# Optimization experiments

Hardware: AMD Instinct MI355X
Metric: run time of the kernel (lower is better)

Reference implementation:

```python
import jax, jax.numpy as jnp
import numpy as np

N_HEADS = 16


def setup_inputs() -> dict:
    key = jax.random.key(0)
    ks = jax.random.split(key, 5)
    E = 1024
    x = jax.random.normal(ks[0], (2, 2048, E), dtype=jnp.float32)
    s = 1.0 / np.sqrt(E)
    Wq = jax.random.normal(ks[1], (E, E), dtype=jnp.float32) * s
    Wk = jax.random.normal(ks[2], (E, E), dtype=jnp.float32) * s
    Wv = jax.random.normal(ks[3], (E, E), dtype=jnp.float32) * s
    Wo = jax.random.normal(ks[4], (E, E), dtype=jnp.float32) * s
    bo = jnp.zeros((E,), dtype=jnp.float32)
    return {"x": x, "Wq": Wq, "Wk": Wk, "Wv": Wv, "Wo": Wo, "bo": bo}


def reference(x, Wq, Wk, Wv, Wo, bo):
    B, S, E = x.shape
    H = N_HEADS
    D = E // H
    # project and split heads: [B, H, S, D]
    def split_heads(y):
        return y.reshape(B, S, H, D).transpose(0, 2, 1, 3)
    q = split_heads(x @ Wq)
    k = split_heads(x @ Wk)
    v = split_heads(x @ Wv)
    # full score matrix [B, H, S, S]
    scores = jnp.einsum('bhqd,bhkd->bhqk', q, k)
    causal = jnp.triu(jnp.ones((S, S), dtype=bool), k=1)
    scores = jnp.where(causal, -jnp.inf, scores)
    attn = jax.nn.softmax(scores / jnp.sqrt(jnp.float32(D)), axis=-1)
    # dropout rate is 0.0 -> identity
    ctx = jnp.einsum('bhqk,bhkd->bhqd', attn, v)
    ctx = ctx.transpose(0, 2, 1, 3).reshape(B, S, E)
    return ctx @ Wo + bo
```

## Files before the change

### kernel.cpp

```cpp
#include <hip/hip_runtime.h>
#include <stdint.h>


#define N_HEADS 16
#define HD 64
#define SEQ 2048
#define EMB 1024

typedef __attribute__((ext_vector_type(8))) short s16x8;
typedef __attribute__((ext_vector_type(4))) float f32x4;
typedef __attribute__((ext_vector_type(16))) float f32x16;

#define QSCALE 0.18033688f

__device__ __forceinline__ short f2b(float f) {
  union { float f; uint32_t u; } v; v.f = f;
  uint32_t u = v.u;
  u += 0x7fffu + ((u >> 16) & 1u);
  return (short)(u >> 16);
}

__device__ __forceinline__ uint32_t pk2(float a, float b) {
  union { float f; uint32_t u; } x, y; x.f = a; y.f = b;
  return ((x.u + 0x8000u) >> 16) | ((y.u + 0x8000u) & 0xffff0000u);
}

__device__ __forceinline__ float exp2a(float x) {
  float r; asm("v_exp_f32 %0, %1" : "=v"(r) : "v"(x)); return r;
}

__device__ __forceinline__ void gll16(const void* g, void* l) {
  __builtin_amdgcn_global_load_lds((const __attribute__((address_space(1))) void*)g,
                                   (__attribute__((address_space(3))) void*)l, 16, 0, 0);
}

#define SWZ(row, chunk) ((((row) * 8) + ((chunk) ^ ((row) & 7))) * 8)

__global__ __launch_bounds__(256) void k_prep(const float* __restrict__ x,
                                              const float* __restrict__ W0,
                                              const float* __restrict__ W1,
                                              const float* __restrict__ W2,
                                              const float* __restrict__ W3,
                                              short* __restrict__ xb,
                                              short* __restrict__ wt) {
  const int z = blockIdx.x, t = threadIdx.x;
  if (z < 4096) {
    int i = z * 256 + t;
    float4 v = ((const float4*)x)[i];
    short4 o;
    o.x = f2b(v.x); o.y = f2b(v.y); o.z = f2b(v.z); o.w = f2b(v.w);
    ((short4*)xb)[i] = o;
  } else {
    __shared__ float tile[32][33];
    int bz = z - 4096;
    int w = bz >> 10, rem = bz & 1023;
    int bn = (rem & 31) * 32, bk = (rem >> 5) * 32;
    const float* W = w == 0 ? W0 : w == 1 ? W1 : w == 2 ? W2 : W3;
    short* o = wt + (size_t)w * EMB * EMB;
    int tx = t & 31, ty = t >> 5;
    for (int i = ty; i < 32; i += 8)
      tile[i][tx] = W[(size_t)(bk + i) * EMB + bn + tx];
    __syncthreads();
    for (int i = ty; i < 32; i += 8)
      o[(size_t)(bn + i) * EMB + bk + tx] = f2b(tile[tx][i]);
  }
}

template <int MODE>
__global__ __launch_bounds__(256) void k_gemm(const short* __restrict__ A,
                                              const short* __restrict__ BT,
                                              void* __restrict__ outp,
                                              const float* __restrict__ bias) {
  constexpr bool SWAP = (MODE != 2);
  constexpr int MAIN = 4 * 4096;
  constexpr int EPIL = (MODE == 1) ? 0 : 128 * 132;
  constexpr int SMSZ = MAIN > EPIL ? MAIN : EPIL;
  __shared__ alignas(16) short smem[SMSZ];

  const int t = threadIdx.x;
  const int m0 = blockIdx.x * 128;
  const int n0 = blockIdx.y * 128;
  const int wave = t >> 6, lane = t & 63;
  const int wm = (wave >> 1) * 64, wn = (wave & 1) * 64;
  const int l31 = lane & 31, lh = lane >> 5;

  const int srow = lane >> 2;
  const int soff = ((lane & 3) ^ (srow & 3)) * 8;

  auto stage = [&](int kb, int p) {
    short* as = smem + p * 4096;
    short* bs = smem + 8192 + p * 4096;
#pragma unroll
    for (int i = 0; i < 2; i++) {
      int rb = wave * 32 + i * 16;
      gll16(A + (size_t)(m0 + rb + srow) * EMB + kb + soff, &as[rb * 32]);
      gll16(BT + (size_t)(n0 + rb + srow) * EMB + kb + soff, &bs[rb * 32]);
    }
  };
  auto frd = [&](const short* sb, int row, int kh) -> s16x8 {
    int c = kh * 2 + lh;
    return *(const s16x8*)&sb[row * 32 + ((c ^ (row & 3)) * 8)];
  };

  f32x16 acc[2][2] = {};
  int pb = 0;
  stage(0, 0);
  for (int kb = 0; kb < EMB; kb += 32) {
    __syncthreads();
    if (kb + 32 < EMB) stage(kb + 32, pb ^ 1);
    const short* as = smem + pb * 4096;
    const short* bs = smem + 8192 + pb * 4096;
    s16x8 af[2][2], bf[2][2];
#pragma unroll
    for (int mt = 0; mt < 2; mt++)
#pragma unroll
      for (int kh = 0; kh < 2; kh++) af[mt][kh] = frd(as, wm + mt * 32 + l31, kh);
#pragma unroll
    for (int nt = 0; nt < 2; nt++)
#pragma unroll
      for (int kh = 0; kh < 2; kh++) bf[nt][kh] = frd(bs, wn + nt * 32 + l31, kh);
#pragma unroll
    for (int mt = 0; mt < 2; mt++)
#pragma unroll
      for (int nt = 0; nt < 2; nt++)
#pragma unroll
        for (int kh = 0; kh < 2; kh++)
          acc[mt][nt] = SWAP
            ? __builtin_amdgcn_mfma_f32_32x32x16_bf16(bf[nt][kh], af[mt][kh], acc[mt][nt], 0, 0, 0)
            : __builtin_amdgcn_mfma_f32_32x32x16_bf16(af[mt][kh], bf[nt][kh], acc[mt][nt], 0, 0, 0);
    pb ^= 1;
  }

  if (MODE == 0) {
    __syncthreads();
    short* Vls = smem;
    const int wsel = blockIdx.y >> 3;
    const float qs = (wsel == 0) ? QSCALE : 1.0f;
    const int n0l = (blockIdx.y & 7) * 128;
#pragma unroll
    for (int mt = 0; mt < 2; mt++) {
      int mr = wm + mt * 32 + l31;
#pragma unroll
      for (int nt = 0; nt < 2; nt++)
#pragma unroll
        for (int g = 0; g < 4; g++) {
          uint2 w;
          w.x = pk2(acc[mt][nt][4 * g + 0] * qs, acc[mt][nt][4 * g + 1] * qs);
          w.y = pk2(acc[mt][nt][4 * g + 2] * qs, acc[mt][nt][4 * g + 3] * qs);
          *(uint2*)&Vls[mr * 132 + wn + nt * 32 + g * 8 + 4 * lh] = w;
        }
    }
    __syncthreads();
    short* ob = (short*)outp + (size_t)wsel * (4u * 1024 * 1024);
    const int bb = m0 >> 11, ss0 = m0 & (SEQ - 1);
#pragma unroll
    for (int i = 0; i < 8; i++) {
      int mrow = i * 16 + (t >> 4);
      int ncol = (t & 15) * 8;
      int e = n0l + ncol, hh = e >> 6, dd = e & 63;
      *(uint4*)&ob[(((size_t)(bb * N_HEADS + hh) * SEQ) + ss0 + mrow) * 64 + dd] =
          *(const uint4*)&Vls[mrow * 132 + ncol];
    }
  } else if (MODE == 2) {
    __syncthreads();
    short* Vls = smem;
#pragma unroll
    for (int nt = 0; nt < 2; nt++) {
      int nl = wn + nt * 32 + l31;
#pragma unroll
      for (int mt = 0; mt < 2; mt++)
#pragma unroll
        for (int g = 0; g < 4; g++) {
          uint2 w;
          w.x = pk2(acc[mt][nt][4 * g + 0], acc[mt][nt][4 * g + 1]);
          w.y = pk2(acc[mt][nt][4 * g + 2], acc[mt][nt][4 * g + 3]);
          *(uint2*)&Vls[nl * 132 + wm + mt * 32 + g * 8 + 4 * lh] = w;
        }
    }
    __syncthreads();
    short* obv = (short*)outp + (size_t)8 * 1024 * 1024;
    const int bb = m0 >> 11, ss0 = m0 & (SEQ - 1);
#pragma unroll
    for (int i = 0; i < 8; i++) {
      int nl = i * 16 + (t >> 4);
      int mc = (t & 15) * 8;
      int e = n0 + nl, hh = e >> 6, dd = e & 63;
      *(uint4*)&obv[((size_t)((bb * N_HEADS + hh) * HD + dd)) * SEQ + ss0 + mc] =
          *(const uint4*)&Vls[nl * 132 + mc];
    }
  } else {
    float* of = (float*)outp;
#pragma unroll
    for (int mt = 0; mt < 2; mt++) {
      int mg = m0 + wm + mt * 32 + l31;
#pragma unroll
      for (int nt = 0; nt < 2; nt++)
#pragma unroll
        for (int g = 0; g < 4; g++) {
          int ng = n0 + wn + nt * 32 + g * 8 + 4 * lh;
          f32x4 bv = *(const f32x4*)&bias[ng];
          f32x4 w;
          w[0] = acc[mt][nt][4 * g + 0] + bv[0];
          w[1] = acc[mt][nt][4 * g + 1] + bv[1];
          w[2] = acc[mt][nt][4 * g + 2] + bv[2];
          w[3] = acc[mt][nt][4 * g + 3] + bv[3];
          *(f32x4*)&of[(size_t)mg * EMB + ng] = w;
        }
    }
  }
}

__global__ __launch_bounds__(256) void k_attn(const short* __restrict__ Q,
                                              const short* __restrict__ K,
                                              const short* __restrict__ Vt,
                                              short* __restrict__ ctx) {
  __shared__ alignas(16) short UQP[64 * 72];
  __shared__ alignas(16) short Ks0[64 * 64], Ks1[64 * 64];
  __shared__ alignas(16) short Vs0[64 * 64], Vs1[64 * 64];

  const int t = threadIdx.x, wave = t >> 6, lane = t & 63;
  const int ml = lane & 15, quad = lane >> 4;
  const int bh = blockIdx.x;
  const int qb = 31 - (int)blockIdx.y;
  const size_t base = (size_t)bh * SEQ * HD;
  const int q0 = qb * 64, wq = q0 + wave * 16;

  const int sr = lane >> 3;
  const int sc = ((lane & 7) ^ sr) * 8;

#pragma unroll
  for (int i = 0; i < 2; i++) {
    int r8 = wave * 16 + i * 8;
    gll16(Q + base + (size_t)(q0 + r8 + sr) * HD + sc, &UQP[r8 * 64]);
  }
  auto stageKV = [&](int kt, short* kd, short* vd) {
    const int kbase = kt * 64;
#pragma unroll
    for (int i = 0; i < 2; i++) {
      int r8 = wave * 16 + i * 8;
      gll16(K + base + (size_t)(kbase + r8 + sr) * HD + sc, &kd[r8 * 64]);
      gll16(Vt + base + (size_t)(r8 + sr) * SEQ + kbase + sc, &vd[r8 * 64]);
    }
  };

  f32x4 cacc[4] = {};
  float li = 0.f;
  short* Pw = &UQP[wave * 16 * 72];

  stageKV(0, Ks0, Vs0);
  __syncthreads();

  s16x8 qf[2];
#pragma unroll
  for (int c = 0; c < 2; c++)
    qf[c] = *(const s16x8*)&UQP[SWZ(wave * 16 + ml, 4 * c + quad)];
  __syncthreads();

  auto tile_body = [&](int kt, const short* kd, const short* vd) {
    const int kbase = kt * 64;
    if (kbase > wq + 15) return;
    const bool diag = (kbase + 63 > wq);
    f32x4 st[4];
#pragma unroll
    for (int nt = 0; nt < 4; nt++) {
      int row = nt * 16 + ml;
      s16x8 kf0 = *(const s16x8*)&kd[SWZ(row, quad)];
      s16x8 kf1 = *(const s16x8*)&kd[SWZ(row, 4 + quad)];
      f32x4 z = {};
      z = __builtin_amdgcn_mfma_f32_16x16x32_bf16(kf0, qf[0], z, 0, 0, 0);
      st[nt] = __builtin_amdgcn_mfma_f32_16x16x32_bf16(kf1, qf[1], z, 0, 0, 0);
    }
    const int qg = wq + ml;
    float rsum = 0.f;
#pragma unroll
    for (int nt = 0; nt < 4; nt++) {
      float p0 = exp2a(st[nt][0]);
      float p1 = exp2a(st[nt][1]);
      float p2 = exp2a(st[nt][2]);
      float p3 = exp2a(st[nt][3]);
      if (diag) {
        int kk = kbase + nt * 16 + quad * 4;
        if (kk + 0 > qg) p0 = 0.f;
        if (kk + 1 > qg) p1 = 0.f;
        if (kk + 2 > qg) p2 = 0.f;
        if (kk + 3 > qg) p3 = 0.f;
      }
      rsum += (p0 + p1) + (p2 + p3);
      uint2 w; w.x = pk2(p0, p1); w.y = pk2(p2, p3);
      *(uint2*)&Pw[ml * 72 + nt * 16 + quad * 4] = w;
    }
    li += rsum;
    __builtin_amdgcn_wave_barrier();

    s16x8 pf[2];
#pragma unroll
    for (int c = 0; c < 2; c++)
      pf[c] = *(const s16x8*)&Pw[ml * 72 + c * 32 + quad * 8];
#pragma unroll
    for (int mt = 0; mt < 4; mt++) {
      int row = mt * 16 + ml;
      s16x8 vf0 = *(const s16x8*)&vd[SWZ(row, quad)];
      s16x8 vf1 = *(const s16x8*)&vd[SWZ(row, 4 + quad)];
      cacc[mt] = __builtin_amdgcn_mfma_f32_16x16x32_bf16(vf0, pf[0], cacc[mt], 0, 0, 0);
      cacc[mt] = __builtin_amdgcn_mfma_f32_16x16x32_bf16(vf1, pf[1], cacc[mt], 0, 0, 0);
    }
  };

  for (int kt = 0; kt <= qb; kt += 2) {
    if (kt + 1 <= qb) stageKV(kt + 1, Ks1, Vs1);
    tile_body(kt, Ks0, Vs0);
    __syncthreads();
    if (kt + 2 <= qb) stageKV(kt + 2, Ks0, Vs0);
    if (kt + 1 <= qb) tile_body(kt + 1, Ks1, Vs1);
    __syncthreads();
  }

  li += __shfl_xor(li, 16, 64);
  li += __shfl_xor(li, 32, 64);
  float inv = 1.0f / li;
#pragma unroll
  for (int mt = 0; mt < 4; mt++) {
    uint2 w;
    w.x = pk2(cacc[mt][0] * inv, cacc[mt][1] * inv);
    w.y = pk2(cacc[mt][2] * inv, cacc[mt][3] * inv);
    *(uint2*)&Pw[ml * 72 + mt * 16 + quad * 4] = w;
  }
  __builtin_amdgcn_wave_barrier();
  const int b = bh >> 4, h = bh & 15;
#pragma unroll
  for (int i = 0; i < 2; i++) {
    int row = i * 8 + (lane >> 3);
    int q = wq + row;
    size_t gbase = ((size_t)(b * SEQ + q)) * EMB + h * 64 + (lane & 7) * 8;
    *(uint4*)&ctx[gbase] = *(const uint4*)&Pw[row * 72 + (lane & 7) * 8];
  }
}

extern "C" void kernel_launch(void* const* d_in, const int* in_sizes, int n_in,
                              void* d_out, int out_size, void* d_ws, size_t ws_size,
                              hipStream_t stream) {
  const float* x  = (const float*)d_in[0];
  const float* Wq = (const float*)d_in[1];
  const float* Wk = (const float*)d_in[2];
  const float* Wv = (const float*)d_in[3];
  const float* Wo = (const float*)d_in[4];
  const float* bo = (const float*)d_in[5];
  float* out = (float*)d_out;

  short* ws = (short*)d_ws;
  short* xb  = ws;
  short* wt  = ws + (size_t)4 * 1024 * 1024;
  short* qkv = ws + (size_t)8 * 1024 * 1024;

  k_prep<<<8192, 256, 0, stream>>>(x, Wq, Wk, Wv, Wo, xb, wt);
  k_gemm<0><<<dim3(32, 16), 256, 0, stream>>>(xb, wt, qkv, nullptr);
  k_gemm<2><<<dim3(32, 8), 256, 0, stream>>>(xb, wt + (size_t)2 * 1024 * 1024, qkv, nullptr);
  k_attn<<<dim3(32, 32), 256, 0, stream>>>(qkv, qkv + (size_t)4 * 1024 * 1024,
                                           qkv + (size_t)8 * 1024 * 1024, xb);
  k_gemm<1><<<dim3(32, 8), 256, 0, stream>>>(xb, wt + (size_t)3 * 1024 * 1024, out, bo);
}
```

Before: 179.6 us.

## Fuse QKV projections into one launch and use 128-row query blocks in attention

Merges the Q/K projection GEMM and the transposed V projection GEMM into a single launch with 24 column blocks, choosing the MFMA operand order and epilogue per block at runtime. The attention kernel now uses 512 threads per block covering 128 query rows, so each staged K/V tile serves twice as many queries and the grid is halved. This cuts one kernel launch and halves the K/V reloads. In exchange there are fewer attention blocks to spread over the compute units, and the causal work per block is less even.

```diff
diff --git a/kernel.cpp b/kernel.cpp
--- a/kernel.cpp
+++ b/kernel.cpp
@@ -12,6 +12,8 @@
 typedef __attribute__((ext_vector_type(16))) float f32x16;
 
 #define QSCALE 0.18033688f
+
+template <bool B> struct BC { static constexpr bool value = B; };
 
 __device__ __forceinline__ short f2b(float f) {
   union { float f; uint32_t u; } v; v.f = f;
@@ -71,15 +73,15 @@
                                               const short* __restrict__ BT,
                                               void* __restrict__ outp,
                                               const float* __restrict__ bias) {
-  constexpr bool SWAP = (MODE != 2);
   constexpr int MAIN = 4 * 4096;
   constexpr int EPIL = (MODE == 1) ? 0 : 128 * 132;
   constexpr int SMSZ = MAIN > EPIL ? MAIN : EPIL;
   __shared__ alignas(16) short smem[SMSZ];
 
   const int t = threadIdx.x;
+  const int by = blockIdx.y;
   const int m0 = blockIdx.x * 128;
-  const int n0 = blockIdx.y * 128;
+  const short* Bp = BT + (size_t)by * (128 * EMB);
   const int wave = t >> 6, lane = t & 63;
   const int wm = (wave >> 1) * 64, wn = (wave & 1) * 64;
   const int l31 = lane & 31, lh = lane >> 5;
@@ -94,7 +96,7 @@
     for (int i = 0; i < 2; i++) {
       int rb = wave * 32 + i * 16;
       gll16(A + (size_t)(m0 + rb + srow) * EMB + kb + soff, &as[rb * 32]);
-      gll16(BT + (size_t)(n0 + rb + srow) * EMB + kb + soff, &bs[rb * 32]);
+      gll16(Bp + (size_t)(rb + srow) * EMB + kb + soff, &bs[rb * 32]);
     }
   };
   auto frd = [&](const short* sb, int row, int kh) -> s16x8 {
@@ -103,93 +105,104 @@
   };
 
   f32x16 acc[2][2] = {};
-  int pb = 0;
-  stage(0, 0);
-  for (int kb = 0; kb < EMB; kb += 32) {
-    __syncthreads();
-    if (kb + 32 < EMB) stage(kb + 32, pb ^ 1);
-    const short* as = smem + pb * 4096;
-    const short* bs = smem + 8192 + pb * 4096;
-    s16x8 af[2][2], bf[2][2];
-#pragma unroll
-    for (int mt = 0; mt < 2; mt++)
-#pragma unroll
-      for (int kh = 0; kh < 2; kh++) af[mt][kh] = frd(as, wm + mt * 32 + l31, kh);
-#pragma unroll
-    for (int nt = 0; nt < 2; nt++)
-#pragma unroll
-      for (int kh = 0; kh < 2; kh++) bf[nt][kh] = frd(bs, wn + nt * 32 + l31, kh);
-#pragma unroll
-    for (int mt = 0; mt < 2; mt++)
+
+  auto kloop = [&](auto SWC) {
+    constexpr bool SW = decltype(SWC)::value;
+    int pb = 0;
+    stage(0, 0);
+    for (int kb = 0; kb < EMB; kb += 32) {
+      __syncthreads();
+      if (kb + 32 < EMB) stage(kb + 32, pb ^ 1);
+      const short* as = smem + pb * 4096;
+      const short* bs = smem + 8192 + pb * 4096;
+      s16x8 af[2][2], bf[2][2];
+#pragma unroll
+      for (int mt = 0; mt < 2; mt++)
+#pragma unroll
+        for (int kh = 0; kh < 2; kh++) af[mt][kh] = frd(as, wm + mt * 32 + l31, kh);
 #pragma unroll
       for (int nt = 0; nt < 2; nt++)
 #pragma unroll
-        for (int kh = 0; kh < 2; kh++)
-          acc[mt][nt] = SWAP
-            ? __builtin_amdgcn_mfma_f32_32x32x16_bf16(bf[nt][kh], af[mt][kh], acc[mt][nt], 0, 0, 0)
-            : __builtin_amdgcn_mfma_f32_32x32x16_bf16(af[mt][kh], bf[nt][kh], acc[mt][nt], 0, 0, 0);
-    pb ^= 1;
-  }
+        for (int kh = 0; kh < 2; kh++) bf[nt][kh] = frd(bs, wn + nt * 32 + l31, kh);
+#pragma unroll
+      for (int mt = 0; mt < 2; mt++)
+#pragma unroll
+        for (int nt = 0; nt < 2; nt++)
+#pragma unroll
+          for (int kh = 0; kh < 2; kh++)
+            acc[mt][nt] = SW
+              ? __builtin_amdgcn_mfma_f32_32x32x16_bf16(bf[nt][kh], af[mt][kh], acc[mt][nt], 0, 0, 0)
+              : __builtin_amdgcn_mfma_f32_32x32x16_bf16(af[mt][kh], bf[nt][kh], acc[mt][nt], 0, 0, 0);
+      pb ^= 1;
+    }
+  };
+
+  if (MODE == 1 || by < 16) kloop(BC<true>{});
+  else                      kloop(BC<false>{});
 
   if (MODE == 0) {
-    __syncthreads();
-    short* Vls = smem;
-    const int wsel = blockIdx.y >> 3;
-    const float qs = (wsel == 0) ? QSCALE : 1.0f;
-    const int n0l = (blockIdx.y & 7) * 128;
-#pragma unroll
-    for (int mt = 0; mt < 2; mt++) {
-      int mr = wm + mt * 32 + l31;
-#pragma unroll
-      for (int nt = 0; nt < 2; nt++)
-#pragma unroll
-        for (int g = 0; g < 4; g++) {
-          uint2 w;
-          w.x = pk2(acc[mt][nt][4 * g + 0] * qs, acc[mt][nt][4 * g + 1] * qs);
-          w.y = pk2(acc[mt][nt][4 * g + 2] * qs, acc[mt][nt][4 * g + 3] * qs);
-          *(uint2*)&Vls[mr * 132 + wn + nt * 32 + g * 8 + 4 * lh] = w;
-        }
-    }
-    __syncthreads();
-    short* ob = (short*)outp + (size_t)wsel * (4u * 1024 * 1024);
-    const int bb = m0 >> 11, ss0 = m0 & (SEQ - 1);
-#pragma unroll
-    for (int i = 0; i < 8; i++) {
-      int mrow = i * 16 + (t >> 4);
-      int ncol = (t & 15) * 8;
-      int e = n0l + ncol, hh = e >> 6, dd = e & 63;
-      *(uint4*)&ob[(((size_t)(bb * N_HEADS + hh) * SEQ) + ss0 + mrow) * 64 + dd] =
-          *(const uint4*)&Vls[mrow * 132 + ncol];
-    }
-  } else if (MODE == 2) {
-    __syncthreads();
-    short* Vls = smem;
-#pragma unroll
-    for (int nt = 0; nt < 2; nt++) {
-      int nl = wn + nt * 32 + l31;
-#pragma unroll
-      for (int mt = 0; mt < 2; mt++)
-#pragma unroll
-        for (int g = 0; g < 4; g++) {
-          uint2 w;
-          w.x = pk2(acc[mt][nt][4 * g + 0], acc[mt][nt][4 * g + 1]);
-          w.y = pk2(acc[mt][nt][4 * g + 2], acc[mt][nt][4 * g + 3]);
-          *(uint2*)&Vls[nl * 132 + wm + mt * 32 + g * 8 + 4 * lh] = w;
-        }
-    }
-    __syncthreads();
-    short* obv = (short*)outp + (size_t)8 * 1024 * 1024;
-    const int bb = m0 >> 11, ss0 = m0 & (SEQ - 1);
-#pragma unroll
-    for (int i = 0; i < 8; i++) {
-      int nl = i * 16 + (t >> 4);
-      int mc = (t & 15) * 8;
-      int e = n0 + nl, hh = e >> 6, dd = e & 63;
-      *(uint4*)&obv[((size_t)((bb * N_HEADS + hh) * HD + dd)) * SEQ + ss0 + mc] =
-          *(const uint4*)&Vls[nl * 132 + mc];
+    if (by < 16) {
+      __syncthreads();
+      short* Vls = smem;
+      const int wsel = by >> 3;
+      const float qs = (wsel == 0) ? QSCALE : 1.0f;
+      const int n0l = (by & 7) * 128;
+#pragma unroll
+      for (int mt = 0; mt < 2; mt++) {
+        int mr = wm + mt * 32 + l31;
+#pragma unroll
+        for (int nt = 0; nt < 2; nt++)
+#pragma unroll
+          for (int g = 0; g < 4; g++) {
+            uint2 w;
+            w.x = pk2(acc[mt][nt][4 * g + 0] * qs, acc[mt][nt][4 * g + 1] * qs);
+            w.y = pk2(acc[mt][nt][4 * g + 2] * qs, acc[mt][nt][4 * g + 3] * qs);
+            *(uint2*)&Vls[mr * 132 + wn + nt * 32 + g * 8 + 4 * lh] = w;
+          }
+      }
+      __syncthreads();
+      short* ob = (short*)outp + (size_t)wsel * (4u * 1024 * 1024);
+      const int bb = m0 >> 11, ss0 = m0 & (SEQ - 1);
+#pragma unroll
+      for (int i = 0; i < 8; i++) {
+        int mrow = i * 16 + (t >> 4);
+        int ncol = (t & 15) * 8;
+        int e = n0l + ncol, hh = e >> 6, dd = e & 63;
+        *(uint4*)&ob[(((size_t)(bb * N_HEADS + hh) * SEQ) + ss0 + mrow) * 64 + dd] =
+            *(const uint4*)&Vls[mrow * 132 + ncol];
+      }
+    } else {
+      __syncthreads();
+      short* Vls = smem;
+#pragma unroll
+      for (int nt = 0; nt < 2; nt++) {
+        int nl = wn + nt * 32 + l31;
+#pragma unroll
+        for (int mt = 0; mt < 2; mt++)
+#pragma unroll
+          for (int g = 0; g < 4; g++) {
+            uint2 w;
+            w.x = pk2(acc[mt][nt][4 * g + 0], acc[mt][nt][4 * g + 1]);
+            w.y = pk2(acc[mt][nt][4 * g + 2], acc[mt][nt][4 * g + 3]);
+            *(uint2*)&Vls[nl * 132 + wm + mt * 32 + g * 8 + 4 * lh] = w;
+          }
+      }
+      __syncthreads();
+      short* obv = (short*)outp + (size_t)8 * 1024 * 1024;
+      const int n0l = (by & 7) * 128;
+      const int bb = m0 >> 11, ss0 = m0 & (SEQ - 1);
+#pragma unroll
+      for (int i = 0; i < 8; i++) {
+        int nl = i * 16 + (t >> 4);
+        int mc = (t & 15) * 8;
+        int e = n0l + nl, hh = e >> 6, dd = e & 63;
+        *(uint4*)&obv[((size_t)((bb * N_HEADS + hh) * HD + dd)) * SEQ + ss0 + mc] =
+            *(const uint4*)&Vls[nl * 132 + mc];
+      }
     }
   } else {
     float* of = (float*)outp;
+    const int n0 = by * 128;
 #pragma unroll
     for (int mt = 0; mt < 2; mt++) {
       int mg = m0 + wm + mt * 32 + l31;
@@ -210,20 +223,20 @@
   }
 }
 
-__global__ __launch_bounds__(256) void k_attn(const short* __restrict__ Q,
+__global__ __launch_bounds__(512) void k_attn(const short* __restrict__ Q,
                                               const short* __restrict__ K,
                                               const short* __restrict__ Vt,
                                               short* __restrict__ ctx) {
-  __shared__ alignas(16) short UQP[64 * 72];
+  __shared__ alignas(16) short UQP[128 * 72];
   __shared__ alignas(16) short Ks0[64 * 64], Ks1[64 * 64];
   __shared__ alignas(16) short Vs0[64 * 64], Vs1[64 * 64];
 
   const int t = threadIdx.x, wave = t >> 6, lane = t & 63;
   const int ml = lane & 15, quad = lane >> 4;
   const int bh = blockIdx.x;
-  const int qb = 31 - (int)blockIdx.y;
+  const int qb = 15 - (int)blockIdx.y;
   const size_t base = (size_t)bh * SEQ * HD;
-  const int q0 = qb * 64, wq = q0 + wave * 16;
+  const int q0 = qb * 128, wq = q0 + wave * 16;
 
   const int sr = lane >> 3;
   const int sc = ((lane & 7) ^ sr) * 8;
@@ -235,12 +248,9 @@
   }
   auto stageKV = [&](int kt, short* kd, short* vd) {
     const int kbase = kt * 64;
-#pragma unroll
-    for (int i = 0; i < 2; i++) {
-      int r8 = wave * 16 + i * 8;
-      gll16(K + base + (size_t)(kbase + r8 + sr) * HD + sc, &kd[r8 * 64]);
-      gll16(Vt + base + (size_t)(r8 + sr) * SEQ + kbase + sc, &vd[r8 * 64]);
-    }
+    const int r8 = wave * 8;
+    gll16(K + base + (size_t)(kbase + r8 + sr) * HD + sc, &kd[r8 * 64]);
+    gll16(Vt + base + (size_t)(r8 + sr) * SEQ + kbase + sc, &vd[r8 * 64]);
   };
 
   f32x4 cacc[4] = {};
@@ -306,12 +316,13 @@
     }
   };
 
-  for (int kt = 0; kt <= qb; kt += 2) {
-    if (kt + 1 <= qb) stageKV(kt + 1, Ks1, Vs1);
+  const int nkt = 2 * qb + 2;
+  for (int kt = 0; kt < nkt; kt += 2) {
+    stageKV(kt + 1, Ks1, Vs1);
     tile_body(kt, Ks0, Vs0);
     __syncthreads();
-    if (kt + 2 <= qb) stageKV(kt + 2, Ks0, Vs0);
-    if (kt + 1 <= qb) tile_body(kt + 1, Ks1, Vs1);
+    if (kt + 2 < nkt) stageKV(kt + 2, Ks0, Vs0);
+    tile_body(kt + 1, Ks1, Vs1);
     __syncthreads();
   }
 
@@ -353,9 +364,8 @@
   short* qkv = ws + (size_t)8 * 1024 * 1024;
 
   k_prep<<<8192, 256, 0, stream>>>(x, Wq, Wk, Wv, Wo, xb, wt);
-  k_gemm<0><<<dim3(32, 16), 256, 0, stream>>>(xb, wt, qkv, nullptr);
-  k_gemm<2><<<dim3(32, 8), 256, 0, stream>>>(xb, wt + (size_t)2 * 1024 * 1024, qkv, nullptr);
-  k_attn<<<dim3(32, 32), 256, 0, stream>>>(qkv, qkv + (size_t)4 * 1024 * 1024,
+  k_gemm<0><<<dim3(32, 24), 256, 0, stream>>>(xb, wt, qkv, nullptr);
+  k_attn<<<dim3(32, 16), 512, 0, stream>>>(qkv, qkv + (size_t)4 * 1024 * 1024,
                                            qkv + (size_t)8 * 1024 * 1024, xb);
   k_gemm<1><<<dim3(32, 8), 256, 0, stream>>>(xb, wt + (size_t)3 * 1024 * 1024, out, bo);
 }
```

Measured after the change: 172.6 us. 1.04x faster.
